# Kernel tuning notes

Hardware: AMD Instinct MI355X
Metric: run time of the kernel (lower is better)

## Reference

```python
import jax, jax.numpy as jnp
import numpy as np
import math

ALPHA = 2.0  # spikingjelly surrogate.ATan default alpha
TAU = 2.0
MEM_DECAY = math.exp(-1.0 / TAU)
ADAPT_STRENGTH = 0.1
TARGET_RATE = 0.02
THR_MIN = 0.5
N_HEAD = 4

@jax.custom_vjp
def spike_fn(x):
    # Heaviside forward, ATan surrogate backward
    return (x >= 0.0).astype(x.dtype)

def _spike_fwd(x):
    return spike_fn(x), x

def _spike_bwd(x, g):
    return (g * (ALPHA / 2.0) / (1.0 + (jnp.pi / 2.0 * ALPHA * x) ** 2),)

spike_fn.defvjp(_spike_fwd, _spike_bwd)

def lif_step(x, v_mem, thr):
    # thr is a buffer in torch (updated under no_grad): no grad flows to it
    thr_c = jax.lax.stop_gradient(thr)
    v_pot = v_mem * MEM_DECAY + x
    spike = spike_fn(v_pot - thr_c)
    v_new = v_pot * (1.0 - jax.lax.stop_gradient(spike))
    err = jax.lax.stop_gradient(jnp.mean(spike)) - TARGET_RATE
    thr_new = jnp.maximum(thr_c + ADAPT_STRENGTH * err, THR_MIN)
    return spike, v_new, thr_new

def setup_inputs() -> dict:
    key = jax.random.key(0)
    ks = jax.random.split(key, 10)
    B, T, S, D, DS = 8, 16, 256, 512, 64
    x = jax.random.normal(ks[0], (B, T, S, D), jnp.float32)
    A = jax.random.normal(ks[1], (DS, DS), jnp.float32)
    C = jax.random.normal(ks[2], (D, DS), jnp.float32)
    s = 1.0 / math.sqrt(DS)
    Wq = jax.random.uniform(ks[3], (DS, DS), jnp.float32, -s, s)
    bq = jax.random.uniform(ks[4], (DS,), jnp.float32, -s, s)
    sd = 1.0 / math.sqrt(D)
    Wkv = jax.random.uniform(ks[5], (2 * DS, D), jnp.float32, -sd, sd)
    bkv = jax.random.uniform(ks[6], (2 * DS,), jnp.float32, -sd, sd)
    Wo = jax.random.uniform(ks[7], (DS, DS), jnp.float32, -s, s)
    bo = jax.random.uniform(ks[8], (DS,), jnp.float32, -s, s)
    thr_s0 = jnp.full((DS,), 1.0, jnp.float32)
    thr_o0 = jnp.full((D,), 1.0, jnp.float32)
    return {"x": x, "A": A, "C": C, "Wq": Wq, "bq": bq, "Wkv": Wkv,
            "bkv": bkv, "Wo": Wo, "bo": bo, "thr_s0": thr_s0, "thr_o0": thr_o0}

def reference(x, A, C, Wq, bq, Wkv, bkv, Wo, bo, thr_s0, thr_o0):
    B, T, S, D = x.shape
    DS = A.shape[0]
    H = N_HEAD
    dh = DS // H
    N = B * S
    scale = 1.0 / math.sqrt(dh)
    h0 = jnp.zeros((B, S, DS), x.dtype)
    sv0 = jnp.zeros((B, S, DS), x.dtype)
    ov0 = jnp.zeros((B, S, D), x.dtype)

    def step(carry, x_t):
        h, sv, ov, ts, to = carry
        state_transition = h @ A.T                              # (B,S,DS)
        q = (h @ Wq.T + bq).reshape(N, H, dh).transpose(1, 0, 2)   # (H,N,dh)
        kv = x_t @ Wkv.T + bkv                                  # (B,S,2*DS)
        k = kv[..., :DS].reshape(N, H, dh).transpose(1, 0, 2)   # (H,N,dh)
        v = kv[..., DS:].reshape(N, H, dh).transpose(1, 0, 2)   # (H,N,dh)
        scores = jnp.einsum('hnd,hmd->hnm', q, k) * scale       # (H,N,N)
        w = jax.nn.softmax(scores, axis=-1)
        att = jnp.einsum('hnm,hmd->hnd', w, v)                  # (H,N,dh)
        att = att.transpose(1, 0, 2).reshape(B, S, DS)
        state_update = state_transition + att @ Wo.T + bo
        h2, sv2, ts2 = lif_step(state_update, sv, ts)
        output_potential = h2 @ C.T                             # (B,S,D)
        out, ov2, to2 = lif_step(output_potential, ov, to)
        return (h2, sv2, ov2, ts2, to2), out

    _, outs = jax.lax.scan(step, (h0, sv0, ov0, thr_s0, thr_o0),
                           jnp.moveaxis(x, 1, 0))               # outs: (T,B,S,D)
    return jnp.moveaxis(outs, 0, 1)                             # (B,T,S,D)
```

## Files before the change

### kernel.cpp

```cpp
#include <hip/hip_runtime.h>
#include <math.h>


#define NTOK   2048
#define TSTEPS 16
#define NSPLIT 32

#define MEMDECAY ((float)0.6065306597126334)
#define SCALE    0.25f
#define LOG2E    1.4426950408889634f

#define OFF_KV   ((size_t)0)
#define OFF_PACC ((size_t)4194304)
#define OFF_OV   ((size_t)8388608)
#define OFF_H    ((size_t)9437184)
#define OFF_SV   ((size_t)9568256)
#define OFF_Q    ((size_t)9699328)
#define OFF_PM   ((size_t)9830400)
#define OFF_PL   ((size_t)10092544)
#define OFF_CT   ((size_t)10354688)
#define OFF_CNT  ((size_t)10387456)
#define OFF_WT   ((size_t)10387488)

__global__ __launch_bounds__(256) void init_kernel(const float* __restrict__ bq,
                                                   const float* __restrict__ C,
                                                   const float* __restrict__ Wkv,
                                                   float* __restrict__ ws) {
  int i = blockIdx.x * 256 + threadIdx.x;
  if (i < 327680) {
    float4 z = {0.f, 0.f, 0.f, 0.f};
    ((float4*)(ws + OFF_OV))[i] = z;
    return;
  }
  i -= 327680;
  if (i < 131072) { ws[OFF_Q + i] = bq[i & 63]; return; }
  i -= 131072;
  if (i < 32768) {
    int k = i >> 9, c = i & 511;
    ws[OFF_CT + i] = C[c * 64 + k];
    return;
  }
  i -= 32768;
  if (i < 65536) {
    int k = i >> 7, o = i & 127;
    ws[OFF_WT + i] = Wkv[o * 512 + k];
    return;
  }
  i -= 65536;
  if (i < 32) ((int*)(ws + OFF_CNT))[i] = 0;
}

__global__ __launch_bounds__(256) void kv_gemm_kernel(const float* __restrict__ x,
                                                      const float* __restrict__ wkt,
                                                      const float* __restrict__ bkv,
                                                      float* __restrict__ ws) {
  __shared__ float xs[64 * 68];
  __shared__ float wt[64 * 136];
  const int tid = threadIdx.x;
  const int mbase = blockIdx.x * 64;
  const int rg = tid >> 4;
  const int cg = tid & 15;

  float acc[4][8];
#pragma unroll
  for (int i = 0; i < 4; ++i)
#pragma unroll
    for (int j = 0; j < 8; ++j) acc[i][j] = 0.f;

  for (int kt = 0; kt < 8; ++kt) {
    const int kb = kt * 64;
#pragma unroll
    for (int p = 0; p < 4; ++p) {
      int e = tid + p * 256;
      int r = e >> 4, kq = e & 15;
      int row = mbase + r;
      int t_ = row >> 11, n = row & 2047;
      int b = n >> 8, s = n & 255;
      float4 v = *(const float4*)(x + (size_t)((b * 16 + t_) * 256 + s) * 512 + kb + kq * 4);
      *(float4*)(xs + r * 68 + kq * 4) = v;
    }
#pragma unroll
    for (int p = 0; p < 8; ++p) {
      int e = tid + p * 256;
      int k = e >> 5, cq = e & 31;
      float4 v = *(const float4*)(wkt + (size_t)(kb + k) * 128 + cq * 4);
      *(float4*)(wt + k * 136 + cq * 4) = v;
    }
    __syncthreads();
#pragma unroll 2
    for (int kq = 0; kq < 16; ++kq) {
      float4 a0 = *(const float4*)(xs + (rg * 4 + 0) * 68 + kq * 4);
      float4 a1 = *(const float4*)(xs + (rg * 4 + 1) * 68 + kq * 4);
      float4 a2 = *(const float4*)(xs + (rg * 4 + 2) * 68 + kq * 4);
      float4 a3 = *(const float4*)(xs + (rg * 4 + 3) * 68 + kq * 4);
      const float* ap[4] = {(const float*)&a0, (const float*)&a1,
                            (const float*)&a2, (const float*)&a3};
#pragma unroll
      for (int kk = 0; kk < 4; ++kk) {
        const float* wp = wt + (kq * 4 + kk) * 136 + cg * 8;
        float4 b0 = *(const float4*)(wp);
        float4 b1 = *(const float4*)(wp + 4);
#pragma unroll
        for (int i = 0; i < 4; ++i) {
          float av = ap[i][kk];
          acc[i][0] += av * b0.x; acc[i][1] += av * b0.y;
          acc[i][2] += av * b0.z; acc[i][3] += av * b0.w;
          acc[i][4] += av * b1.x; acc[i][5] += av * b1.y;
          acc[i][6] += av * b1.z; acc[i][7] += av * b1.w;
        }
      }
    }
    __syncthreads();
  }
  float4 bb0 = *(const float4*)(bkv + cg * 8);
  float4 bb1 = *(const float4*)(bkv + cg * 8 + 4);
  float* kvout = ws + OFF_KV;
#pragma unroll
  for (int i = 0; i < 4; ++i) {
    float* op = kvout + (size_t)(mbase + rg * 4 + i) * 128 + cg * 8;
    float4 v0; v0.x = acc[i][0] + bb0.x; v0.y = acc[i][1] + bb0.y;
    v0.z = acc[i][2] + bb0.z; v0.w = acc[i][3] + bb0.w;
    float4 v1; v1.x = acc[i][4] + bb1.x; v1.y = acc[i][5] + bb1.y;
    v1.z = acc[i][6] + bb1.z; v1.w = acc[i][7] + bb1.w;
    *(float4*)(op) = v0;
    *(float4*)(op + 4) = v1;
  }
}

__device__ __forceinline__ void attp_body(int blk, int tid, int t,
                                          const float* __restrict__ kvbase,
                                          const float* __restrict__ qbuf,
                                          float* __restrict__ pm,
                                          float* __restrict__ pl,
                                          float* __restrict__ pacc,
                                          float* smem) {
  const int head = blk & 3;
  const int qt = (blk >> 2) & 3;
  const int sp = blk >> 4;
  float* kl = smem;
  float* vl = smem + 1024;
  const float* kvt = kvbase + (size_t)t * NTOK * 128;
  {
    int key = tid >> 2, dq = tid & 3;
    const float* base = kvt + (size_t)(sp * 64 + key) * 128 + head * 16;
    float4 kk = ((const float4*)base)[dq];
    float4 vv = ((const float4*)(base + 64))[dq];
    ((float4*)kl)[key * 4 + dq] = kk;
    ((float4*)vl)[key * 4 + dq] = vv;
  }
  const int i0 = qt * 512 + tid;
  const int i1 = i0 + 256;
  float q0[16], q1[16];
  {
    const float4* qp0 = (const float4*)(qbuf + (size_t)i0 * 64 + head * 16);
    const float4* qp1 = (const float4*)(qbuf + (size_t)i1 * 64 + head * 16);
#pragma unroll
    for (int r = 0; r < 4; ++r) {
      float4 a = qp0[r];
      q0[4 * r] = a.x; q0[4 * r + 1] = a.y; q0[4 * r + 2] = a.z; q0[4 * r + 3] = a.w;
      float4 b = qp1[r];
      q1[4 * r] = b.x; q1[4 * r + 1] = b.y; q1[4 * r + 2] = b.z; q1[4 * r + 3] = b.w;
    }
  }
  __syncthreads();
  float m0 = -INFINITY, l0 = 0.f, m1 = -INFINITY, l1 = 0.f;
  float acc0[16], acc1[16];
#pragma unroll
  for (int d = 0; d < 16; ++d) { acc0[d] = 0.f; acc1[d] = 0.f; }

#pragma unroll
  for (int ch = 0; ch < 4; ++ch) {
    float sc0[16], sc1[16];
#pragma unroll
    for (int j = 0; j < 16; ++j) {
      const float* kp = kl + (ch * 16 + j) * 16;
      float s0 = 0.f, s1 = 0.f;
#pragma unroll
      for (int d = 0; d < 16; ++d) { float kv_ = kp[d]; s0 += q0[d] * kv_; s1 += q1[d] * kv_; }
      sc0[j] = s0 * SCALE; sc1[j] = s1 * SCALE;
    }
    float mb0 = sc0[0], mb1 = sc1[0];
#pragma unroll
    for (int j = 1; j < 16; ++j) { mb0 = fmaxf(mb0, sc0[j]); mb1 = fmaxf(mb1, sc1[j]); }
    float mn0 = fmaxf(m0, mb0), mn1 = fmaxf(m1, mb1);
    float r0 = exp2f((m0 - mn0) * LOG2E), r1 = exp2f((m1 - mn1) * LOG2E);
    l0 *= r0; l1 *= r1;
#pragma unroll
    for (int d = 0; d < 16; ++d) { acc0[d] *= r0; acc1[d] *= r1; }
#pragma unroll
    for (int j = 0; j < 16; ++j) {
      float w0 = exp2f((sc0[j] - mn0) * LOG2E), w1 = exp2f((sc1[j] - mn1) * LOG2E);
      l0 += w0; l1 += w1; sc0[j] = w0; sc1[j] = w1;
    }
#pragma unroll
    for (int j = 0; j < 16; ++j) {
      const float* vp = vl + (ch * 16 + j) * 16;
      float w0 = sc0[j], w1 = sc1[j];
#pragma unroll
      for (int d = 0; d < 16; ++d) { float vv = vp[d]; acc0[d] += w0 * vv; acc1[d] += w1 * vv; }
    }
    m0 = mn0; m1 = mn1;
  }
  const int pbase = (head * NSPLIT + sp) * NTOK;
  pm[pbase + i0] = m0; pm[pbase + i1] = m1;
  pl[pbase + i0] = l0; pl[pbase + i1] = l1;
  float4* pa0 = (float4*)(pacc + (size_t)(pbase + i0) * 16);
  float4* pa1 = (float4*)(pacc + (size_t)(pbase + i1) * 16);
#pragma unroll
  for (int r = 0; r < 4; ++r) {
    float4 v0; v0.x = acc0[4 * r]; v0.y = acc0[4 * r + 1]; v0.z = acc0[4 * r + 2]; v0.w = acc0[4 * r + 3];
    pa0[r] = v0;
    float4 v1; v1.x = acc1[4 * r]; v1.y = acc1[4 * r + 1]; v1.z = acc1[4 * r + 2]; v1.w = acc1[4 * r + 3];
    pa1[r] = v1;
  }
}

__global__ __launch_bounds__(256) void attp_kernel(int t, float* __restrict__ ws) {
  __shared__ float smem[2048];
  attp_body(blockIdx.x, threadIdx.x, t, ws + OFF_KV, ws + OFF_Q,
            ws + OFF_PM, ws + OFF_PL, ws + OFF_PACC, smem);
}

__global__ __launch_bounds__(256) void combine_lifs_kernel(
    int t, const float* __restrict__ A, const float* __restrict__ Wq,
    const float* __restrict__ bq, const float* __restrict__ Wo,
    const float* __restrict__ bo, const float* __restrict__ thr_s0,
    float* __restrict__ ws) {
  __shared__ float As[64 * 68], Wqs[64 * 68], Wos[64 * 68];
  __shared__ float att_s[4][64];
  __shared__ int scnt;
  const int tid = threadIdx.x;
#pragma unroll
  for (int p = 0; p < 4; ++p) {
    int e = tid + p * 256;
    int c = e >> 4, kq = e & 15;
    *(float4*)(As + c * 68 + kq * 4)  = *(const float4*)(A + c * 64 + kq * 4);
    *(float4*)(Wqs + c * 68 + kq * 4) = *(const float4*)(Wq + c * 64 + kq * 4);
    *(float4*)(Wos + c * 68 + kq * 4) = *(const float4*)(Wo + c * 64 + kq * 4);
  }
  if (tid == 0) scnt = 0;

  const float* pm = ws + OFF_PM;
  const float* pl = ws + OFF_PL;
  const float* pacc = ws + OFF_PACC;
  float* h = ws + OFF_H;
  float* sv = ws + OFF_SV;
  float* qb = ws + OFF_Q;
  int* cnt = (int*)(ws + OFF_CNT);

  const int lane = tid & 63, w = tid >> 6;
  const int n = blockIdx.x * 4 + w;
  const int head = lane >> 4, d = lane & 15;
  const int pb = head * NSPLIT * NTOK + n;

  float mstar = -INFINITY;
  for (int s = 0; s < NSPLIT; ++s) mstar = fmaxf(mstar, pm[pb + s * NTOK]);
  float lst = 0.f, av = 0.f;
  for (int s = 0; s < NSPLIT; ++s) {
    float e = exp2f((pm[pb + s * NTOK] - mstar) * LOG2E);
    lst += e * pl[pb + s * NTOK];
    av += e * pacc[(size_t)(pb + s * NTOK) * 16 + d];
  }
  att_s[w][lane] = av / lst;
  float hv = h[n * 64 + lane];
  unsigned long long hm = __ballot(hv > 0.5f);
  __syncthreads();

  float st = 0.f;
  {
    unsigned long long m = hm;
    while (m) {
      int k = __builtin_ctzll(m);
      m &= m - 1;
      st += As[lane * 68 + k];
    }
  }
  const float* Wor = Wos + lane * 68;
  float wo = 0.f;
#pragma unroll
  for (int kq = 0; kq < 16; ++kq) {
    float4 wb = *(const float4*)(Wor + kq * 4);
    float4 ab = *(const float4*)(&att_s[w][kq * 4]);
    wo += ab.x * wb.x; wo += ab.y * wb.y; wo += ab.z * wb.z; wo += ab.w * wb.w;
  }
  float su = st + wo + bo[lane];

  float thr = thr_s0[0];
  const float inv = 1.0f / 131072.0f;
  for (int i = 0; i < t; ++i) {
    float mean = (float)cnt[i] * inv;
    thr = fmaxf(thr + 0.1f * (mean - 0.02f), 0.5f);
  }
  float svo = sv[n * 64 + lane];
  float vpot = svo * MEMDECAY + su;
  float spk = (vpot >= thr) ? 1.f : 0.f;
  h[n * 64 + lane] = spk;
  sv[n * 64 + lane] = vpot * (1.f - spk);
  unsigned long long sm = __ballot(spk > 0.5f);

  float qv = 0.f;
  {
    unsigned long long m = sm;
    while (m) {
      int k = __builtin_ctzll(m);
      m &= m - 1;
      qv += Wqs[lane * 68 + k];
    }
  }
  qb[n * 64 + lane] = qv + bq[lane];

  if (lane == 0) atomicAdd(&scnt, __popcll(sm));
  __syncthreads();
  if (tid == 0) atomicAdd(&cnt[t], scnt);
}

__global__ __launch_bounds__(256) void fused_out_attp_kernel(
    int t, const float* __restrict__ thr_o0, float* __restrict__ out,
    float* __restrict__ ws) {
  __shared__ float smem[64 * 68 + 64 * 68];
  __shared__ int scnt;
  const int blk = blockIdx.x;
  if (blk >= 256) {
    attp_body(blk - 256, threadIdx.x, t + 1, ws + OFF_KV, ws + OFF_Q,
              ws + OFF_PM, ws + OFF_PL, ws + OFF_PACC, smem);
    return;
  }
  const int tid = threadIdx.x;
  const int nt = blk >> 3;
  const int ct = blk & 7;
  float* hs = smem;
  float* cts = smem + 64 * 68;
  const float* h = ws + OFF_H;
  const float* Ct = ws + OFF_CT;
  float* ov = ws + OFF_OV;
  int* cnt = (int*)(ws + OFF_CNT);

#pragma unroll
  for (int p = 0; p < 4; ++p) {
    int e = tid + p * 256;
    int r = e >> 4, kq = e & 15;
    float4 v = *(const float4*)(h + (size_t)(nt * 64 + r) * 64 + kq * 4);
    *(float4*)(hs + r * 68 + kq * 4) = v;
  }
#pragma unroll
  for (int p = 0; p < 4; ++p) {
    int e = tid + p * 256;
    int k = e >> 4, cq = e & 15;
    float4 v = *(const float4*)(Ct + (size_t)k * 512 + ct * 64 + cq * 4);
    *(float4*)(cts + k * 68 + cq * 4) = v;
  }
  if (tid == 0) scnt = 0;
  __syncthreads();

  const int tr = tid >> 4, tc = tid & 15;
  float acc[4][4];
#pragma unroll
  for (int i = 0; i < 4; ++i)
#pragma unroll
    for (int j = 0; j < 4; ++j) acc[i][j] = 0.f;

#pragma unroll 4
  for (int k4 = 0; k4 < 16; ++k4) {
    float4 hv[4];
#pragma unroll
    for (int i = 0; i < 4; ++i) hv[i] = *(const float4*)(hs + (tr + i * 16) * 68 + k4 * 4);
#pragma unroll
    for (int kk = 0; kk < 4; ++kk) {
      float4 c = *(const float4*)(cts + (k4 * 4 + kk) * 68 + tc * 4);
#pragma unroll
      for (int i = 0; i < 4; ++i) {
        float hvv = ((const float*)&hv[i])[kk];
        acc[i][0] += hvv * c.x;
        acc[i][1] += hvv * c.y;
        acc[i][2] += hvv * c.z;
        acc[i][3] += hvv * c.w;
      }
    }
  }

  float thr = thr_o0[0];
  const float inv = 1.0f / 1048576.0f;
  for (int i = 0; i < t; ++i) {
    float mean = (float)cnt[16 + i] * inv;
    thr = fmaxf(thr + 0.1f * (mean - 0.02f), 0.5f);
  }

  int mycount = 0;
#pragma unroll
  for (int i = 0; i < 4; ++i) {
    int n = nt * 64 + tr + i * 16;
    int b = n >> 8, s = n & 255;
    size_t coff = (size_t)ct * 64 + tc * 4;
    float* ovp = ov + (size_t)n * 512 + coff;
    float* outp = out + ((size_t)(b * 16 + t) * 256 + s) * 512 + coff;
    float4 o = *(float4*)ovp;
    float v0 = o.x * MEMDECAY + acc[i][0];
    float v1 = o.y * MEMDECAY + acc[i][1];
    float v2 = o.z * MEMDECAY + acc[i][2];
    float v3 = o.w * MEMDECAY + acc[i][3];
    float s0 = (v0 >= thr) ? 1.f : 0.f;
    float s1 = (v1 >= thr) ? 1.f : 0.f;
    float s2 = (v2 >= thr) ? 1.f : 0.f;
    float s3 = (v3 >= thr) ? 1.f : 0.f;
    float4 sp; sp.x = s0; sp.y = s1; sp.z = s2; sp.w = s3;
    *(float4*)outp = sp;
    float4 nv; nv.x = v0 * (1.f - s0); nv.y = v1 * (1.f - s1);
    nv.z = v2 * (1.f - s2); nv.w = v3 * (1.f - s3);
    *(float4*)ovp = nv;
    mycount += (int)(s0 + s1 + s2 + s3);
  }
  atomicAdd(&scnt, mycount);
  __syncthreads();
  if (tid == 0) atomicAdd(&cnt[16 + t], scnt);
}

extern "C" void kernel_launch(void* const* d_in, const int* in_sizes, int n_in,
                              void* d_out, int out_size, void* d_ws, size_t ws_size,
                              hipStream_t stream) {
  const float* x    = (const float*)d_in[0];
  const float* A    = (const float*)d_in[1];
  const float* C    = (const float*)d_in[2];
  const float* Wq   = (const float*)d_in[3];
  const float* bq   = (const float*)d_in[4];
  const float* Wkv  = (const float*)d_in[5];
  const float* bkv  = (const float*)d_in[6];
  const float* Wo   = (const float*)d_in[7];
  const float* bo   = (const float*)d_in[8];
  const float* th_s = (const float*)d_in[9];
  const float* th_o = (const float*)d_in[10];
  float* out = (float*)d_out;
  float* ws = (float*)d_ws;

  init_kernel<<<dim3(2177), dim3(256), 0, stream>>>(bq, C, Wkv, ws);
  kv_gemm_kernel<<<dim3(512), dim3(256), 0, stream>>>(x, ws + OFF_WT, bkv, ws);
  attp_kernel<<<dim3(512), dim3(256), 0, stream>>>(0, ws);
  for (int t = 0; t < TSTEPS; ++t) {
    combine_lifs_kernel<<<dim3(512), dim3(256), 0, stream>>>(t, A, Wq, bq, Wo, bo, th_s, ws);
    int g = (t < TSTEPS - 1) ? 768 : 256;
    fused_out_attp_kernel<<<dim3(g), dim3(256), 0, stream>>>(t, th_o, out, ws);
  }
}
```

Before: 974.2 us.

## Store hidden spikes as bitmasks and replace output GEMM with sparse column sums

```diff
diff --git a/kernel.cpp b/kernel.cpp
--- a/kernel.cpp
+++ b/kernel.cpp
@@ -21,6 +21,7 @@
 #define OFF_CT   ((size_t)10354688)
 #define OFF_CNT  ((size_t)10387456)
 #define OFF_WT   ((size_t)10387488)
+#define OFF_HM   ((size_t)10453024)
 
 __global__ __launch_bounds__(256) void init_kernel(const float* __restrict__ bq,
                                                    const float* __restrict__ C,
@@ -47,7 +48,12 @@
     return;
   }
   i -= 65536;
-  if (i < 32) ((int*)(ws + OFF_CNT))[i] = 0;
+  if (i < 32) { ((int*)(ws + OFF_CNT))[i] = 0; return; }
+  i -= 32;
+  if (i < 1024) {
+    float4 z = {0.f, 0.f, 0.f, 0.f};
+    ((float4*)(ws + OFF_HM))[i] = z;
+  }
 }
 
 __global__ __launch_bounds__(256) void kv_gemm_kernel(const float* __restrict__ x,
@@ -97,9 +103,9 @@
                             (const float*)&a2, (const float*)&a3};
 #pragma unroll
       for (int kk = 0; kk < 4; ++kk) {
-        const float* wp = wt + (kq * 4 + kk) * 136 + cg * 8;
-        float4 b0 = *(const float4*)(wp);
-        float4 b1 = *(const float4*)(wp + 4);
+        const float* wp = wt + (kq * 4 + kk) * 136;
+        float4 b0 = *(const float4*)(wp + cg * 4);
+        float4 b1 = *(const float4*)(wp + 64 + cg * 4);
 #pragma unroll
         for (int i = 0; i < 4; ++i) {
           float av = ap[i][kk];
@@ -112,18 +118,18 @@
     }
     __syncthreads();
   }
-  float4 bb0 = *(const float4*)(bkv + cg * 8);
-  float4 bb1 = *(const float4*)(bkv + cg * 8 + 4);
+  float4 bb0 = *(const float4*)(bkv + cg * 4);
+  float4 bb1 = *(const float4*)(bkv + 64 + cg * 4);
   float* kvout = ws + OFF_KV;
 #pragma unroll
   for (int i = 0; i < 4; ++i) {
-    float* op = kvout + (size_t)(mbase + rg * 4 + i) * 128 + cg * 8;
+    float* op = kvout + (size_t)(mbase + rg * 4 + i) * 128;
     float4 v0; v0.x = acc[i][0] + bb0.x; v0.y = acc[i][1] + bb0.y;
     v0.z = acc[i][2] + bb0.z; v0.w = acc[i][3] + bb0.w;
     float4 v1; v1.x = acc[i][4] + bb1.x; v1.y = acc[i][5] + bb1.y;
     v1.z = acc[i][6] + bb1.z; v1.w = acc[i][7] + bb1.w;
-    *(float4*)(op) = v0;
-    *(float4*)(op + 4) = v1;
+    *(float4*)(op + cg * 4) = v0;
+    *(float4*)(op + 64 + cg * 4) = v1;
   }
 }
 
@@ -243,10 +249,10 @@
   const float* pm = ws + OFF_PM;
   const float* pl = ws + OFF_PL;
   const float* pacc = ws + OFF_PACC;
-  float* h = ws + OFF_H;
   float* sv = ws + OFF_SV;
   float* qb = ws + OFF_Q;
   int* cnt = (int*)(ws + OFF_CNT);
+  unsigned long long* hmask = (unsigned long long*)(ws + OFF_HM);
 
   const int lane = tid & 63, w = tid >> 6;
   const int n = blockIdx.x * 4 + w;
@@ -262,8 +268,7 @@
     av += e * pacc[(size_t)(pb + s * NTOK) * 16 + d];
   }
   att_s[w][lane] = av / lst;
-  float hv = h[n * 64 + lane];
-  unsigned long long hm = __ballot(hv > 0.5f);
+  unsigned long long hm = hmask[n];
   __syncthreads();
 
   float st = 0.f;
@@ -294,7 +299,6 @@
   float svo = sv[n * 64 + lane];
   float vpot = svo * MEMDECAY + su;
   float spk = (vpot >= thr) ? 1.f : 0.f;
-  h[n * 64 + lane] = spk;
   sv[n * 64 + lane] = vpot * (1.f - spk);
   unsigned long long sm = __ballot(spk > 0.5f);
 
@@ -309,7 +313,10 @@
   }
   qb[n * 64 + lane] = qv + bq[lane];
 
-  if (lane == 0) atomicAdd(&scnt, __popcll(sm));
+  if (lane == 0) {
+    hmask[n] = sm;
+    atomicAdd(&scnt, __popcll(sm));
+  }
   __syncthreads();
   if (tid == 0) atomicAdd(&cnt[t], scnt);
 }
@@ -317,7 +324,7 @@
 __global__ __launch_bounds__(256) void fused_out_attp_kernel(
     int t, const float* __restrict__ thr_o0, float* __restrict__ out,
     float* __restrict__ ws) {
-  __shared__ float smem[64 * 68 + 64 * 68];
+  __shared__ float smem[2048];
   __shared__ int scnt;
   const int blk = blockIdx.x;
   if (blk >= 256) {
@@ -328,56 +335,15 @@
   const int tid = threadIdx.x;
   const int nt = blk >> 3;
   const int ct = blk & 7;
-  float* hs = smem;
-  float* cts = smem + 64 * 68;
-  const float* h = ws + OFF_H;
   const float* Ct = ws + OFF_CT;
   float* ov = ws + OFF_OV;
   int* cnt = (int*)(ws + OFF_CNT);
-
-#pragma unroll
-  for (int p = 0; p < 4; ++p) {
-    int e = tid + p * 256;
-    int r = e >> 4, kq = e & 15;
-    float4 v = *(const float4*)(h + (size_t)(nt * 64 + r) * 64 + kq * 4);
-    *(float4*)(hs + r * 68 + kq * 4) = v;
-  }
-#pragma unroll
-  for (int p = 0; p < 4; ++p) {
-    int e = tid + p * 256;
-    int k = e >> 4, cq = e & 15;
-    float4 v = *(const float4*)(Ct + (size_t)k * 512 + ct * 64 + cq * 4);
-    *(float4*)(cts + k * 68 + cq * 4) = v;
-  }
+  const unsigned long long* hmask = (const unsigned long long*)(ws + OFF_HM);
+
   if (tid == 0) scnt = 0;
   __syncthreads();
 
   const int tr = tid >> 4, tc = tid & 15;
-  float acc[4][4];
-#pragma unroll
-  for (int i = 0; i < 4; ++i)
-#pragma unroll
-    for (int j = 0; j < 4; ++j) acc[i][j] = 0.f;
-
-#pragma unroll 4
-  for (int k4 = 0; k4 < 16; ++k4) {
-    float4 hv[4];
-#pragma unroll
-    for (int i = 0; i < 4; ++i) hv[i] = *(const float4*)(hs + (tr + i * 16) * 68 + k4 * 4);
-#pragma unroll
-    for (int kk = 0; kk < 4; ++kk) {
-      float4 c = *(const float4*)(cts + (k4 * 4 + kk) * 68 + tc * 4);
-#pragma unroll
-      for (int i = 0; i < 4; ++i) {
-        float hvv = ((const float*)&hv[i])[kk];
-        acc[i][0] += hvv * c.x;
-        acc[i][1] += hvv * c.y;
-        acc[i][2] += hvv * c.z;
-        acc[i][3] += hvv * c.w;
-      }
-    }
-  }
-
   float thr = thr_o0[0];
   const float inv = 1.0f / 1048576.0f;
   for (int i = 0; i < t; ++i) {
@@ -389,15 +355,23 @@
 #pragma unroll
   for (int i = 0; i < 4; ++i) {
     int n = nt * 64 + tr + i * 16;
+    size_t coff = (size_t)ct * 64 + tc * 4;
+    float a0 = 0.f, a1 = 0.f, a2 = 0.f, a3 = 0.f;
+    unsigned long long m = hmask[n];
+    while (m) {
+      int k = __builtin_ctzll(m);
+      m &= m - 1;
+      float4 c = *(const float4*)(Ct + (size_t)k * 512 + coff);
+      a0 += c.x; a1 += c.y; a2 += c.z; a3 += c.w;
+    }
     int b = n >> 8, s = n & 255;
-    size_t coff = (size_t)ct * 64 + tc * 4;
     float* ovp = ov + (size_t)n * 512 + coff;
     float* outp = out + ((size_t)(b * 16 + t) * 256 + s) * 512 + coff;
     float4 o = *(float4*)ovp;
-    float v0 = o.x * MEMDECAY + acc[i][0];
-    float v1 = o.y * MEMDECAY + acc[i][1];
-    float v2 = o.z * MEMDECAY + acc[i][2];
-    float v3 = o.w * MEMDECAY + acc[i][3];
+    float v0 = o.x * MEMDECAY + a0;
+    float v1 = o.y * MEMDECAY + a1;
+    float v2 = o.z * MEMDECAY + a2;
+    float v3 = o.w * MEMDECAY + a3;
     float s0 = (v0 >= thr) ? 1.f : 0.f;
     float s1 = (v1 >= thr) ? 1.f : 0.f;
     float s2 = (v2 >= thr) ? 1.f : 0.f;
@@ -431,7 +405,7 @@
   float* out = (float*)d_out;
   float* ws = (float*)d_ws;
 
-  init_kernel<<<dim3(2177), dim3(256), 0, stream>>>(bq, C, Wkv, ws);
+  init_kernel<<<dim3(2181), dim3(256), 0, stream>>>(bq, C, Wkv, ws);
   kv_gemm_kernel<<<dim3(512), dim3(256), 0, stream>>>(x, ws + OFF_WT, bkv, ws);
   attp_kernel<<<dim3(512), dim3(256), 0, stream>>>(0, ws);
   for (int t = 0; t < TSTEPS; ++t) {
```

Result: faster. 910.3 us (-6.6%).
